# Kernel optimization log

Measured on AMD Instinct MI355X. Metric: run time of the kernel, lower is better.

The kernel has to match this reference:

```python
import jax, jax.numpy as jnp
import numpy as np

B, S, HLEN, VLEN, HID = 32, 2048, 1024, 1024, 1024


def setup_inputs() -> dict:
    key = jax.random.key(0)
    ks = jax.random.split(key, 6)
    scale_W = 1.0 / np.sqrt(HLEN)
    scale_U = 1.0 / np.sqrt(VLEN)
    scale_w = 1.0 / np.sqrt(HID)
    return {
        "h": jax.random.normal(ks[0], (B, HLEN), dtype=jnp.float32),
        "V": jax.random.normal(ks[1], (B, S, VLEN), dtype=jnp.float32),
        "W_w": jax.random.normal(ks[2], (HID, HLEN), dtype=jnp.float32) * scale_W,
        "W_b": jax.random.normal(ks[3], (HID,), dtype=jnp.float32) * scale_W,
        "U_w": jax.random.normal(ks[4], (HID, VLEN), dtype=jnp.float32) * scale_U,
        "w_w": jax.random.normal(ks[5], (HID,), dtype=jnp.float32) * scale_w,
    }


def reference(h, V, W_w, W_b, U_w, w_w):
    # e = w^T tanh(W h + U V^T + b); beta = softmax(e); out = sum_s beta_s V_s
    h_proj = h @ W_w.T + W_b                      # [B, HID]
    V_proj = jnp.einsum('bsv,dv->bsd', V, U_w)    # [B, S, HID]
    e = jnp.einsum('bsd,d->bs', jnp.tanh(h_proj[:, None, :] + V_proj), w_w)  # [B, S]
    beta = jax.nn.softmax(e, axis=1)              # [B, S]
    return jnp.einsum('bs,bsv->bv', beta, V)      # [B, VLEN]
```

## Files before the change

### kernel.cpp

```cpp
#include <hip/hip_runtime.h>

constexpr int B_   = 32;
constexpr int S_   = 2048;
constexpr int HID_ = 1024;
constexpr int VL_  = 1024;

typedef __attribute__((ext_vector_type(4))) float  f32x4;
typedef __attribute__((ext_vector_type(4))) short  s16x4;
typedef __attribute__((ext_vector_type(8))) short  s16x8;

__device__ __forceinline__ short f2bf(float f) {
    union { float f; unsigned u; } v; v.f = f;
    unsigned r = v.u + 0x7fffu + ((v.u >> 16) & 1u);
    return (short)(r >> 16);
}

__device__ __forceinline__ float bf2f(short s) {
    union { unsigned u; float f; } v;
    v.u = ((unsigned)(unsigned short)s) << 16;
    return v.f;
}

__device__ __forceinline__ float fast_tanh(float x) {
    float e2 = __expf(2.0f * x);
    return 1.0f - 2.0f / (e2 + 1.0f);
}

__device__ __forceinline__ void async_cp16(const void* g, void* l) {
    __builtin_amdgcn_global_load_lds(
        (const __attribute__((address_space(1))) unsigned int*)g,
        (__attribute__((address_space(3))) unsigned int*)l,
        16, 0, 0);
}

__global__ __launch_bounds__(256) void hproj_kernel(const float* __restrict__ h,
                                                    const float* __restrict__ Ww,
                                                    const float* __restrict__ Wb,
                                                    float* __restrict__ hp) {
    int tid = threadIdx.x;
    int wave = tid >> 6, lane = tid & 63;
    int d = blockIdx.x * 4 + wave;
    const float* wr = Ww + (size_t)d * HID_;
    float4 wreg[4];
#pragma unroll
    for (int i = 0; i < 4; i++) wreg[i] = *(const float4*)(wr + i * 256 + lane * 4);
    float bias = Wb[d];
    for (int b = 0; b < B_; b++) {
        const float* hr = h + (size_t)b * HID_;
        float acc = 0.0f;
#pragma unroll
        for (int i = 0; i < 4; i++) {
            float4 x = *(const float4*)(hr + i * 256 + lane * 4);
            acc += wreg[i].x * x.x + wreg[i].y * x.y + wreg[i].z * x.z + wreg[i].w * x.w;
        }
#pragma unroll
        for (int o = 32; o; o >>= 1) acc += __shfl_xor(acc, o);
        if (lane == 0) hp[(size_t)b * HID_ + d] = acc + bias;
    }
}

__global__ __launch_bounds__(256) void cvt_kernel(const float* __restrict__ src,
                                                  short* __restrict__ dst, size_t n4) {
    size_t i = (size_t)blockIdx.x * blockDim.x + threadIdx.x;
    size_t stride = (size_t)gridDim.x * blockDim.x;
    for (; i < n4; i += stride) {
        float4 x = ((const float4*)src)[i];
        s16x4 y;
        y.x = f2bf(x.x); y.y = f2bf(x.y); y.z = f2bf(x.z); y.w = f2bf(x.w);
        ((s16x4*)dst)[i] = y;
    }
}

constexpr int BM_E = 256;
constexpr int BK_E = 64;
constexpr int NT_ALL = 4 * (VL_ / BK_E);

__global__ __launch_bounds__(512, 2) void e_kernel_8ph(const short* __restrict__ Vm,
                                                       const short* __restrict__ Um,
                                                       const float* __restrict__ hp,
                                                       const float* __restrict__ ww,
                                                       float* __restrict__ e) {
    __shared__ short Al[2][BM_E][BK_E];
    __shared__ short Bl[2][BM_E][BK_E];

    const int tid  = threadIdx.x;
    const int wave = tid >> 6, lane = tid & 63;
    const int wm = wave >> 2, wn = wave & 3;
    const int col = lane & 15, quad = lane >> 4;
    const int rx  = col & 7;
    const int s0 = blockIdx.x * BM_E;
    const int b  = blockIdx.y;

    const int srow   = lane >> 3;
    const int schunk = (lane & 7) ^ srow;

    const short* gAb = Vm + ((size_t)b * S_ + s0 + wave * 8 + srow) * VL_ + schunk * 8;
    const short* gBb = Um + (size_t)(wave * 8 + srow) * VL_ + schunk * 8;

    float ep[8][4];
#pragma unroll
    for (int i = 0; i < 8; i++)
#pragma unroll
        for (int j = 0; j < 4; j++) ep[i][j] = 0.0f;

    f32x4 acc[8][4];
    f32x4 zero = {0.f, 0.f, 0.f, 0.f};
#pragma unroll
    for (int i = 0; i < 8; i++)
#pragma unroll
        for (int j = 0; j < 4; j++) acc[i][j] = zero;

#pragma unroll
    for (int r = 0; r < 4; ++r) {
        async_cp16(gAb + (size_t)(r * 64) * VL_, &Al[0][r * 64 + wave * 8][0]);
        async_cp16(gBb + (size_t)(r * 64) * VL_, &Bl[0][r * 64 + wave * 8][0]);
    }
    asm volatile("s_waitcnt vmcnt(0)" ::: "memory");
    __builtin_amdgcn_s_barrier();

    for (int T = 0; T < NT_ALL; ++T) {
        const int c  = T & 1;
        const bool pf = (T + 1 < NT_ALL);
        const int ktn = (T + 1) & 15;
        const size_t dtn = (size_t)((T + 1) >> 4);
        const short* gAn = gAb + ktn * BK_E;
        const short* gBn = gBb + (dtn * 256) * VL_ + ktn * BK_E;

        s16x8 b8[4][2];
#pragma unroll
        for (int p = 0; p < 4; ++p) {
            s16x8 a8[2][2];
#pragma unroll
            for (int i = 0; i < 2; ++i)
#pragma unroll
                for (int kk = 0; kk < 2; ++kk)
                    a8[i][kk] = *(const s16x8*)&Al[c][wm * 128 + (2 * p + i) * 16 + col]
                                                    [((((kk << 2) | quad) ^ rx) << 3)];
            if (p == 0) {
#pragma unroll
                for (int tn = 0; tn < 4; ++tn)
#pragma unroll
                    for (int kk = 0; kk < 2; ++kk)
                        b8[tn][kk] = *(const s16x8*)&Bl[c][wn * 64 + tn * 16 + col]
                                                         [((((kk << 2) | quad) ^ rx) << 3)];
            }
            if (pf) {
                if (p == 0) {
                    async_cp16(gBn,                        &Bl[c ^ 1][wave * 8][0]);
                    async_cp16(gBn + (size_t)64 * VL_,     &Bl[c ^ 1][64 + wave * 8][0]);
                } else if (p == 1) {
                    async_cp16(gBn + (size_t)128 * VL_,    &Bl[c ^ 1][128 + wave * 8][0]);
                    async_cp16(gBn + (size_t)192 * VL_,    &Bl[c ^ 1][192 + wave * 8][0]);
                } else if (p == 2) {
                    async_cp16(gAn,                        &Al[c ^ 1][wave * 8][0]);
                    async_cp16(gAn + (size_t)128 * VL_,    &Al[c ^ 1][128 + wave * 8][0]);
                } else {
                    async_cp16(gAn + (size_t)64 * VL_,     &Al[c ^ 1][64 + wave * 8][0]);
                    async_cp16(gAn + (size_t)192 * VL_,    &Al[c ^ 1][192 + wave * 8][0]);
                }
            }
            __builtin_amdgcn_s_barrier();
            __builtin_amdgcn_s_setprio(1);
#pragma unroll
            for (int kk = 0; kk < 2; ++kk)
#pragma unroll
                for (int i = 0; i < 2; ++i)
#pragma unroll
                    for (int tn = 0; tn < 4; ++tn)
                        acc[2 * p + i][tn] = __builtin_amdgcn_mfma_f32_16x16x32_bf16(
                            a8[i][kk], b8[tn][kk], acc[2 * p + i][tn], 0, 0, 0);
            __builtin_amdgcn_s_setprio(0);
            if (p == 1) {
                asm volatile("s_waitcnt vmcnt(4)" ::: "memory");
            } else if (p == 3) {
                if (T == NT_ALL - 2)
                    asm volatile("s_waitcnt vmcnt(0)" ::: "memory");
                else
                    asm volatile("s_waitcnt vmcnt(2)" ::: "memory");
            }
            __builtin_amdgcn_s_barrier();
        }

        if ((T & 15) == 15) {
            const int d0 = (T >> 4) * 256;
            float wv[4], hv[4];
#pragma unroll
            for (int tn = 0; tn < 4; ++tn) {
                int d = d0 + wn * 64 + tn * 16 + col;
                wv[tn] = ww[d];
                hv[tn] = hp[(size_t)b * HID_ + d];
            }
#pragma unroll
            for (int tm = 0; tm < 8; ++tm)
#pragma unroll
                for (int reg = 0; reg < 4; ++reg)
#pragma unroll
                    for (int tn = 0; tn < 4; ++tn)
                        ep[tm][reg] += wv[tn] * fast_tanh(hv[tn] + acc[tm][tn][reg]);
#pragma unroll
            for (int i = 0; i < 8; i++)
#pragma unroll
                for (int j = 0; j < 4; j++) acc[i][j] = zero;
        }
    }

    float* eb = (float*)&Al[0][0][0];
#pragma unroll
    for (int tm = 0; tm < 8; ++tm)
#pragma unroll
        for (int reg = 0; reg < 4; ++reg) {
            float p = ep[tm][reg];
            p += __shfl_xor(p, 1);
            p += __shfl_xor(p, 2);
            p += __shfl_xor(p, 4);
            p += __shfl_xor(p, 8);
            if (col == 0)
                eb[wn * 256 + wm * 128 + tm * 16 + quad * 4 + reg] = p;
        }
    __syncthreads();
    if (tid < 256)
        e[(size_t)b * S_ + s0 + tid] =
            eb[tid] + eb[256 + tid] + eb[512 + tid] + eb[768 + tid];
}

__global__ __launch_bounds__(256) void e_kernel_f32(const float* __restrict__ Vm,
                                                    const float* __restrict__ Um,
                                                    const float* __restrict__ hp,
                                                    const float* __restrict__ ww,
                                                    float* __restrict__ e) {
    __shared__ short As[128][40];
    __shared__ short Bs[128][40];
    int tid = threadIdx.x;
    int b  = blockIdx.z;
    int d0 = blockIdx.x * 128;
    int s0 = blockIdx.y * 128;
    int wave = tid >> 6, lane = tid & 63;
    int wm = wave >> 1, wn = wave & 1;
    int col = lane & 15, quad = lane >> 4;

    f32x4 zero = {0.f, 0.f, 0.f, 0.f};
    f32x4 acc[4][4];
#pragma unroll
    for (int i = 0; i < 4; i++)
#pragma unroll
        for (int j = 0; j < 4; j++) acc[i][j] = zero;

    const float* Abase = Vm + ((size_t)b * S_ + s0) * (size_t)VL_;
    const float* Bbase = Um + (size_t)d0 * (size_t)VL_;

    for (int k0 = 0; k0 < VL_; k0 += 32) {
        int k4 = tid & 7, rb = tid >> 3;
#pragma unroll
        for (int i = 0; i < 4; i++) {
            int r = rb + 32 * i;
            float4 x = *(const float4*)(Abase + (size_t)r * VL_ + k0 + k4 * 4);
            s16x4 ya; ya.x = f2bf(x.x); ya.y = f2bf(x.y); ya.z = f2bf(x.z); ya.w = f2bf(x.w);
            *(s16x4*)&As[r][k4 * 4] = ya;
            float4 y = *(const float4*)(Bbase + (size_t)r * VL_ + k0 + k4 * 4);
            s16x4 yb; yb.x = f2bf(y.x); yb.y = f2bf(y.y); yb.z = f2bf(y.z); yb.w = f2bf(y.w);
            *(s16x4*)&Bs[r][k4 * 4] = yb;
        }
        __syncthreads();
        s16x8 a8[4], b8[4];
#pragma unroll
        for (int tm = 0; tm < 4; tm++)
            a8[tm] = *(const s16x8*)&As[wm * 64 + tm * 16 + col][quad * 8];
#pragma unroll
        for (int tn = 0; tn < 4; tn++)
            b8[tn] = *(const s16x8*)&Bs[wn * 64 + tn * 16 + col][quad * 8];
#pragma unroll
        for (int tm = 0; tm < 4; tm++)
#pragma unroll
            for (int tn = 0; tn < 4; tn++)
                acc[tm][tn] = __builtin_amdgcn_mfma_f32_16x16x32_bf16(
                    a8[tm], b8[tn], acc[tm][tn], 0, 0, 0);
        __syncthreads();
    }

    float wv[4], hv[4];
#pragma unroll
    for (int tn = 0; tn < 4; tn++) {
        int d = d0 + wn * 64 + tn * 16 + col;
        wv[tn] = ww[d];
        hv[tn] = hp[(size_t)b * HID_ + d];
    }
#pragma unroll
    for (int tm = 0; tm < 4; tm++) {
#pragma unroll
        for (int reg = 0; reg < 4; reg++) {
            float p = 0.0f;
#pragma unroll
            for (int tn = 0; tn < 4; tn++)
                p += wv[tn] * fast_tanh(hv[tn] + acc[tm][tn][reg]);
            p += __shfl_xor(p, 1);
            p += __shfl_xor(p, 2);
            p += __shfl_xor(p, 4);
            p += __shfl_xor(p, 8);
            if (col == 0) {
                int s = s0 + wm * 64 + tm * 16 + quad * 4 + reg;
                atomicAdd(&e[(size_t)b * S_ + s], p);
            }
        }
    }
}

__global__ __launch_bounds__(256) void softmax_kernel(const float* __restrict__ epart,
                                                      float* __restrict__ beta,
                                                      int nparts) {
    int b = blockIdx.x, tid = threadIdx.x;
    const float* r0 = epart + (size_t)b * S_;
    const float* r1 = epart + ((size_t)B_ + b) * S_;
    float v[8];
    float m = -1e30f;
#pragma unroll
    for (int i = 0; i < 8; i++) {
        int idx = tid + i * 256;
        v[i] = r0[idx] + (nparts > 1 ? r1[idx] : 0.0f);
        m = fmaxf(m, v[i]);
    }
#pragma unroll
    for (int o = 32; o; o >>= 1) m = fmaxf(m, __shfl_xor(m, o));
    __shared__ float rm[4], rs[4];
    int wave = tid >> 6, lane = tid & 63;
    if (lane == 0) rm[wave] = m;
    __syncthreads();
    m = fmaxf(fmaxf(rm[0], rm[1]), fmaxf(rm[2], rm[3]));
    float s = 0.0f;
#pragma unroll
    for (int i = 0; i < 8; i++) { v[i] = __expf(v[i] - m); s += v[i]; }
#pragma unroll
    for (int o = 32; o; o >>= 1) s += __shfl_xor(s, o);
    if (lane == 0) rs[wave] = s;
    __syncthreads();
    s = rs[0] + rs[1] + rs[2] + rs[3];
    float inv = 1.0f / s;
#pragma unroll
    for (int i = 0; i < 8; i++) beta[(size_t)b * S_ + tid + i * 256] = v[i] * inv;
}

__global__ __launch_bounds__(256) void out_kernel_bf16(const float* __restrict__ beta,
                                                       const short* __restrict__ Vb16,
                                                       float* __restrict__ opart) {
    int b = blockIdx.x, sc = blockIdx.y;
    int v4 = threadIdx.x;
    const short* Vp = Vb16 + ((size_t)b * S_ + (size_t)sc * 128) * VL_;
    const float* bb = beta + (size_t)b * S_ + (size_t)sc * 128;
    float ax = 0.f, ay = 0.f, az = 0.f, aw = 0.f;
    for (int s = 0; s < 128; s++) {
        float w = bb[s];
        s16x4 x = *(const s16x4*)(Vp + (size_t)s * VL_ + v4 * 4);
        ax += w * bf2f(x.x); ay += w * bf2f(x.y);
        az += w * bf2f(x.z); aw += w * bf2f(x.w);
    }
    float4 r = {ax, ay, az, aw};
    *(float4*)(opart + (((size_t)b * 16 + sc) * VL_) + v4 * 4) = r;
}

__global__ __launch_bounds__(256) void out_reduce_kernel(const float* __restrict__ opart,
                                                         float* __restrict__ out) {
    int b = blockIdx.x, v4 = threadIdx.x;
    float4 a = {0.f, 0.f, 0.f, 0.f};
    const float* base = opart + (size_t)b * 16 * VL_;
#pragma unroll
    for (int sc = 0; sc < 16; sc++) {
        float4 x = *(const float4*)(base + (size_t)sc * VL_ + v4 * 4);
        a.x += x.x; a.y += x.y; a.z += x.z; a.w += x.w;
    }
    *(float4*)(out + (size_t)b * VL_ + v4 * 4) = a;
}

__global__ __launch_bounds__(256) void out_kernel_f32(const float* __restrict__ beta,
                                                      const float* __restrict__ V,
                                                      float* __restrict__ out) {
    int b = blockIdx.x, sc = blockIdx.y;
    int v4 = threadIdx.x;
    const float* Vb = V + ((size_t)b * S_ + (size_t)sc * 128) * VL_;
    const float* bb = beta + (size_t)b * S_ + (size_t)sc * 128;
    float ax = 0.f, ay = 0.f, az = 0.f, aw = 0.f;
    for (int s = 0; s < 128; s++) {
        float w = bb[s];
        float4 x = *(const float4*)(Vb + (size_t)s * VL_ + v4 * 4);
        ax += w * x.x; ay += w * x.y; az += w * x.z; aw += w * x.w;
    }
    float* o = out + (size_t)b * VL_ + v4 * 4;
    atomicAdd(o + 0, ax);
    atomicAdd(o + 1, ay);
    atomicAdd(o + 2, az);
    atomicAdd(o + 3, aw);
}

extern "C" void kernel_launch(void* const* d_in, const int* in_sizes, int n_in,
                              void* d_out, int out_size, void* d_ws, size_t ws_size,
                              hipStream_t stream) {
    const float* h  = (const float*)d_in[0];
    const float* V  = (const float*)d_in[1];
    const float* Ww = (const float*)d_in[2];
    const float* Wb = (const float*)d_in[3];
    const float* Uw = (const float*)d_in[4];
    const float* ww = (const float*)d_in[5];
    float* out = (float*)d_out;

    char* ws = (char*)d_ws;
    float* hp    = (float*)ws;
    float* epart = (float*)(ws + 131072);
    float* beta  = (float*)(ws + 131072 + 524288);
    float* opart = (float*)(ws + 131072 + 524288 + 262144);
    size_t fixed = 131072 + 524288 + 262144 + 2097152;
    short* Vb16 = (short*)(ws + fixed);
    short* Ub16 = Vb16 + (size_t)B_ * S_ * VL_;
    size_t need = fixed + ((size_t)B_ * S_ * VL_ + (size_t)HID_ * VL_) * 2;
    bool bf16path = (ws_size >= need);

    hproj_kernel<<<dim3(HID_ / 4), 256, 0, stream>>>(h, Ww, Wb, hp);

    if (bf16path) {
        cvt_kernel<<<4096, 256, 0, stream>>>(V, Vb16, (size_t)B_ * S_ * VL_ / 4);
        cvt_kernel<<<256, 256, 0, stream>>>(Uw, Ub16, (size_t)HID_ * VL_ / 4);
        e_kernel_8ph<<<dim3(S_ / BM_E, B_), 512, 0, stream>>>(Vb16, Ub16, hp, ww, epart);
        softmax_kernel<<<B_, 256, 0, stream>>>(epart, beta, 1);
        out_kernel_bf16<<<dim3(B_, S_ / 128), 256, 0, stream>>>(beta, Vb16, opart);
        out_reduce_kernel<<<B_, 256, 0, stream>>>(opart, out);
    } else {
        hipMemsetAsync(epart, 0, (size_t)B_ * S_ * 4, stream);
        hipMemsetAsync(out, 0, (size_t)out_size * 4, stream);
        e_kernel_f32<<<dim3(HID_ / 128, S_ / 128, B_), 256, 0, stream>>>(
            V, Uw, hp, ww, epart);
        softmax_kernel<<<B_, 256, 0, stream>>>(epart, beta, 1);
        out_kernel_f32<<<dim3(B_, S_ / 128), 256, 0, stream>>>(beta, V, out);
    }
}
```

Before: 596.6 us.

## Fuse V fp32-to-bf16 conversion into first HID block of e kernel

Drops the standalone V conversion kernel. The e kernel now loads fp32 V directly for its first 256-column HID pass, converts it to bf16 in registers, writes it to LDS, and also stores it to the bf16 scratch buffer. Later HID passes and the output kernel read the bf16 scratch as before. This removes one separate full read of V and a kernel launch. In exchange the first pass uses synchronous global loads and extra register pressure instead of async copies, and it relies on the scratch writes being visible to the same block's later async reads.

```diff
diff --git a/kernel.cpp b/kernel.cpp
--- a/kernel.cpp
+++ b/kernel.cpp
@@ -75,11 +75,12 @@
 constexpr int BK_E = 64;
 constexpr int NT_ALL = 4 * (VL_ / BK_E);
 
-__global__ __launch_bounds__(512, 2) void e_kernel_8ph(const short* __restrict__ Vm,
-                                                       const short* __restrict__ Um,
-                                                       const float* __restrict__ hp,
-                                                       const float* __restrict__ ww,
-                                                       float* __restrict__ e) {
+__global__ __launch_bounds__(512, 2) void e_kernel_fused(const float* __restrict__ Vf,
+                                                         const short* __restrict__ Um,
+                                                         const float* __restrict__ hp,
+                                                         const float* __restrict__ ww,
+                                                         float* __restrict__ e,
+                                                         short* __restrict__ Vscr) {
     __shared__ short Al[2][BM_E][BK_E];
     __shared__ short Bl[2][BM_E][BK_E];
 
@@ -94,7 +95,10 @@
     const int srow   = lane >> 3;
     const int schunk = (lane & 7) ^ srow;
 
-    const short* gAb = Vm + ((size_t)b * S_ + s0 + wave * 8 + srow) * VL_ + schunk * 8;
+    const size_t arow = (size_t)b * S_ + s0 + wave * 8 + srow;
+    const float* gAf = Vf   + arow * VL_ + schunk * 8;
+    short*       gAw = Vscr + arow * VL_ + schunk * 8;
+    const short* gAs = Vscr + arow * VL_ + schunk * 8;
     const short* gBb = Um + (size_t)(wave * 8 + srow) * VL_ + schunk * 8;
 
     float ep[8][4];
@@ -111,19 +115,126 @@
         for (int j = 0; j < 4; j++) acc[i][j] = zero;
 
 #pragma unroll
-    for (int r = 0; r < 4; ++r) {
-        async_cp16(gAb + (size_t)(r * 64) * VL_, &Al[0][r * 64 + wave * 8][0]);
+    for (int r = 0; r < 4; ++r)
         async_cp16(gBb + (size_t)(r * 64) * VL_, &Bl[0][r * 64 + wave * 8][0]);
-    }
-    asm volatile("s_waitcnt vmcnt(0)" ::: "memory");
-    __builtin_amdgcn_s_barrier();
-
-    for (int T = 0; T < NT_ALL; ++T) {
+    {
+        float4 fa[4][2];
+#pragma unroll
+        for (int r = 0; r < 4; ++r) {
+            const float* g = gAf + (size_t)(r * 64) * VL_;
+            fa[r][0] = *(const float4*)(g);
+            fa[r][1] = *(const float4*)(g + 4);
+        }
+#pragma unroll
+        for (int r = 0; r < 4; ++r) {
+            s16x8 pk;
+            pk[0] = f2bf(fa[r][0].x); pk[1] = f2bf(fa[r][0].y);
+            pk[2] = f2bf(fa[r][0].z); pk[3] = f2bf(fa[r][0].w);
+            pk[4] = f2bf(fa[r][1].x); pk[5] = f2bf(fa[r][1].y);
+            pk[6] = f2bf(fa[r][1].z); pk[7] = f2bf(fa[r][1].w);
+            *(s16x8*)&Al[0][r * 64 + wave * 8 + srow][(lane & 7) * 8] = pk;
+            *(s16x8*)(gAw + (size_t)(r * 64) * VL_) = pk;
+        }
+    }
+    __syncthreads();
+
+    for (int T = 0; T < 16; ++T) {
+        const int c = T & 1, nb = c ^ 1;
+
+        float4 fa[4][2];
+        if (T < 15) {
+            const float* g0 = gAf + (T + 1) * BK_E;
+#pragma unroll
+            for (int r = 0; r < 4; ++r) {
+                const float* g = g0 + (size_t)(r * 64) * VL_;
+                fa[r][0] = *(const float4*)(g);
+                fa[r][1] = *(const float4*)(g + 4);
+            }
+#pragma unroll
+            for (int r = 0; r < 4; ++r)
+                async_cp16(gBb + (T + 1) * BK_E + (size_t)(r * 64) * VL_,
+                           &Bl[nb][r * 64 + wave * 8][0]);
+        } else {
+#pragma unroll
+            for (int r = 0; r < 4; ++r)
+                async_cp16(gAs + (size_t)(r * 64) * VL_, &Al[nb][r * 64 + wave * 8][0]);
+#pragma unroll
+            for (int r = 0; r < 4; ++r)
+                async_cp16(gBb + (size_t)(256 + r * 64) * VL_,
+                           &Bl[nb][r * 64 + wave * 8][0]);
+        }
+
+        s16x8 b8[4][2];
+#pragma unroll
+        for (int tn = 0; tn < 4; ++tn)
+#pragma unroll
+            for (int kk = 0; kk < 2; ++kk)
+                b8[tn][kk] = *(const s16x8*)&Bl[c][wn * 64 + tn * 16 + col]
+                                                 [((((kk << 2) | quad) ^ rx) << 3)];
+#pragma unroll
+        for (int p = 0; p < 4; ++p) {
+            s16x8 a8[2][2];
+#pragma unroll
+            for (int i = 0; i < 2; ++i)
+#pragma unroll
+                for (int kk = 0; kk < 2; ++kk)
+                    a8[i][kk] = *(const s16x8*)&Al[c][wm * 128 + (2 * p + i) * 16 + col]
+                                                    [((((kk << 2) | quad) ^ rx) << 3)];
+            __builtin_amdgcn_s_setprio(1);
+#pragma unroll
+            for (int kk = 0; kk < 2; ++kk)
+#pragma unroll
+                for (int i = 0; i < 2; ++i)
+#pragma unroll
+                    for (int tn = 0; tn < 4; ++tn)
+                        acc[2 * p + i][tn] = __builtin_amdgcn_mfma_f32_16x16x32_bf16(
+                            a8[i][kk], b8[tn][kk], acc[2 * p + i][tn], 0, 0, 0);
+            __builtin_amdgcn_s_setprio(0);
+        }
+
+        if (T < 15) {
+#pragma unroll
+            for (int r = 0; r < 4; ++r) {
+                s16x8 pk;
+                pk[0] = f2bf(fa[r][0].x); pk[1] = f2bf(fa[r][0].y);
+                pk[2] = f2bf(fa[r][0].z); pk[3] = f2bf(fa[r][0].w);
+                pk[4] = f2bf(fa[r][1].x); pk[5] = f2bf(fa[r][1].y);
+                pk[6] = f2bf(fa[r][1].z); pk[7] = f2bf(fa[r][1].w);
+                *(s16x8*)&Al[nb][r * 64 + wave * 8 + srow][(lane & 7) * 8] = pk;
+                *(s16x8*)(gAw + (T + 1) * BK_E + (size_t)(r * 64) * VL_) = pk;
+            }
+        }
+
+        if (T == 15) {
+            float wv[4], hv[4];
+#pragma unroll
+            for (int tn = 0; tn < 4; ++tn) {
+                int d = wn * 64 + tn * 16 + col;
+                wv[tn] = ww[d];
+                hv[tn] = hp[(size_t)b * HID_ + d];
+            }
+#pragma unroll
+            for (int tm = 0; tm < 8; ++tm)
+#pragma unroll
+                for (int reg = 0; reg < 4; ++reg)
+#pragma unroll
+                    for (int tn = 0; tn < 4; ++tn)
+                        ep[tm][reg] += wv[tn] * fast_tanh(hv[tn] + acc[tm][tn][reg]);
+#pragma unroll
+            for (int i = 0; i < 8; i++)
+#pragma unroll
+                for (int j = 0; j < 4; j++) acc[i][j] = zero;
+        }
+
+        __syncthreads();
+    }
+
+    for (int T = 16; T < NT_ALL; ++T) {
         const int c  = T & 1;
         const bool pf = (T + 1 < NT_ALL);
         const int ktn = (T + 1) & 15;
         const size_t dtn = (size_t)((T + 1) >> 4);
-        const short* gAn = gAb + ktn * BK_E;
+        const short* gAn = gAs + ktn * BK_E;
         const short* gBn = gBb + (dtn * 256) * VL_ + ktn * BK_E;
 
         s16x8 b8[4][2];
@@ -414,9 +525,9 @@
     hproj_kernel<<<dim3(HID_ / 4), 256, 0, stream>>>(h, Ww, Wb, hp);
 
     if (bf16path) {
-        cvt_kernel<<<4096, 256, 0, stream>>>(V, Vb16, (size_t)B_ * S_ * VL_ / 4);
         cvt_kernel<<<256, 256, 0, stream>>>(Uw, Ub16, (size_t)HID_ * VL_ / 4);
-        e_kernel_8ph<<<dim3(S_ / BM_E, B_), 512, 0, stream>>>(Vb16, Ub16, hp, ww, epart);
+        e_kernel_fused<<<dim3(S_ / BM_E, B_), 512, 0, stream>>>(V, Ub16, hp, ww,
+                                                                epart, Vb16);
         softmax_kernel<<<B_, 256, 0, stream>>>(epart, beta, 1);
         out_kernel_bf16<<<dim3(B_, S_ / 128), 256, 0, stream>>>(beta, Vb16, opart);
         out_reduce_kernel<<<B_, 256, 0, stream>>>(opart, out);
```

After: 599.2 us. Within noise of the previous version (+0.4%).
